# Optimization experiments

Hardware: AMD Instinct MI355X
Metric: run time of the kernel (lower is better)

Reference implementation:

```python
import jax, jax.numpy as jnp
import numpy as np

NUM_HEADS = 16
SRC_FACTS = 4


def setup_inputs() -> dict:
    key = jax.random.key(0)
    k1, k2, k3, k4, k5 = jax.random.split(key, 5)
    B, S, H, Dh = 16, 512, NUM_HEADS, 64  # B = batch(4) * src_facts(4)
    D = H * Dh  # d_model = 1024
    pre_q = jax.random.normal(k1, (B, S, H, Dh), dtype=jnp.float32)
    pre_v = jax.random.normal(k2, (B, S, H, Dh), dtype=jnp.float32)
    pre_k = jax.random.normal(k3, (B, S, H, Dh), dtype=jnp.float32)
    attn_mask = jax.random.randint(k4, (B, S, S), 0, 2).astype(jnp.int32)
    output_weights = jax.random.normal(k5, (D, D), dtype=jnp.float32) / np.float32(np.sqrt(D))
    return {
        "pre_q": pre_q,
        "pre_v": pre_v,
        "pre_k": pre_k,
        "attn_mask": attn_mask,
        "output_weights": output_weights,
        "out_seq_len": 512,
        "d_model": 1024,
    }


def reference(pre_q, pre_v, pre_k, attn_mask, output_weights, out_seq_len, d_model):
    B, Sq, H, Dh = pre_q.shape
    # Original: K.sqrt(cast(d_model) // num_heads) -> sqrt(head_dim)
    scale = jnp.sqrt(jnp.float32(float(d_model) // H))
    mask = attn_mask.astype(jnp.float32)[:, None]  # (B, 1, q, k) broadcast over heads
    # scores: (B, H, q, k)
    scores = jnp.einsum("bqhd,bkhd->bhqk", pre_q, pre_k) / scale
    # multiplicative pre-mask + additive -1e9 on masked slots
    scores = scores * mask + (1.0 - mask) * jnp.float32(-1e9)
    # softmax then multiplicative post-mask
    attn = jax.nn.softmax(scores, axis=-1) * mask
    heads = jnp.einsum("bhqk,bkhd->bqhd", attn, pre_v)  # (B, q, H, Dh)
    out = heads.reshape(B, Sq, H * Dh) @ output_weights  # (B, q, d_model)
    return out.reshape(-1, SRC_FACTS, out_seq_len, d_model)
```

## Files before the change

kernel.cpp:

```cpp
#include <hip/hip_runtime.h>
#include <hip/hip_bf16.h>


typedef __bf16 bf16;
typedef bf16 bf16x8 __attribute__((ext_vector_type(8)));
typedef bf16 bf16x4 __attribute__((ext_vector_type(4)));
typedef float floatx4 __attribute__((ext_vector_type(4)));
typedef float floatx16 __attribute__((ext_vector_type(16)));
typedef unsigned short ushort8 __attribute__((ext_vector_type(8)));
typedef unsigned long long u64;

#define MFMA32(A, B, C)  __builtin_amdgcn_mfma_f32_16x16x32_bf16((A), (B), (C), 0, 0, 0)
#define MFMA32x32(A, B, C) __builtin_amdgcn_mfma_f32_32x32x16_bf16((A), (B), (C), 0, 0, 0)

namespace {
constexpr int S   = 512;
constexpr int H   = 16;
constexpr int Dh  = 64;
constexpr int D   = 1024;
constexpr int LDT = 72;
constexpr size_t QN = (size_t)16 * S * H * Dh;
constexpr size_t WN = (size_t)D * D;
}

__device__ __forceinline__ float fexp2(float x) {
#if defined(__HIP_DEVICE_COMPILE__) && __has_builtin(__builtin_amdgcn_exp2f)
    return __builtin_amdgcn_exp2f(x);
#else
    return exp2f(x);
#endif
}

__device__ __forceinline__ int sbfe1(unsigned bits, int bit) {
    return ((int)(bits << (31 - bit))) >> 31;
}

__global__ __launch_bounds__(256)
void prep_kernel(const float* __restrict__ Kf, const float* __restrict__ Vf,
                 const float* __restrict__ Wf, const int* __restrict__ Mg,
                 bf16* __restrict__ Kc, bf16* __restrict__ Vt,
                 bf16* __restrict__ Wt, u64* __restrict__ MB)
{
    __shared__ bf16 Ts[64 * LDT];
    const int blk = blockIdx.x, tid = threadIdx.x;

    if (blk < 4096) {
        const int i = blk * 256 + tid;
        const float* fs = Kf + (size_t)i * 8;
        bf16x8 v;
#pragma unroll
        for (int j = 0; j < 8; ++j) v[j] = (bf16)fs[j];
        *(bf16x8*)(Kc + (size_t)i * 8) = v;
    } else if (blk < 6144) {
        const int bk2 = blk - 4096;
        const int bh  = bk2 >> 3, st = bk2 & 7;
        const int b   = bh >> 4, h = bh & 15;
        const int r   = tid >> 2, c = (tid & 3) * 16;
        const float* src = Vf + ((size_t)((b * S + st * 64 + r) * H + h)) * Dh + c;
#pragma unroll
        for (int i = 0; i < 16; ++i)
            Ts[(c + i) * LDT + r] = (bf16)src[i];
        __syncthreads();
        bf16* dst = Vt + ((size_t)bh * 64 + r) * S + st * 64 + c;
        *(ushort8*)dst       = *(const ushort8*)&Ts[r * LDT + c];
        *(ushort8*)(dst + 8) = *(const ushort8*)&Ts[r * LDT + c + 8];
    } else if (blk < 6400) {
        const int bk2 = blk - 6144;
        const int nb  = bk2 & 15, kb = bk2 >> 4;
        const int r   = tid >> 2, c = (tid & 3) * 16;
        const float* src = Wf + (size_t)(kb * 64 + r) * D + nb * 64 + c;
#pragma unroll
        for (int i = 0; i < 16; ++i)
            Ts[(c + i) * LDT + r] = (bf16)src[i];
        __syncthreads();
        bf16* dst = Wt + (size_t)(nb * 64 + r) * D + kb * 64 + c;
        *(ushort8*)dst       = *(const ushort8*)&Ts[r * LDT + c];
        *(ushort8*)(dst + 8) = *(const ushort8*)&Ts[r * LDT + c + 8];
    } else {
        const int bk2  = blk - 6400;
        const int lane = tid & 63;
        const int idx4 = bk2 * 4 + (tid >> 6);
        const int row  = idx4 >> 1;
        const int half = idx4 & 1;
#pragma unroll
        for (int r = 0; r < 4; ++r) {
            int mv = Mg[(size_t)row * 512 + half * 256 + r * 64 + lane];
            u64 bm = __ballot(mv != 0);
            if (lane == 0) MB[(size_t)row * 8 + half * 4 + r] = bm;
        }
    }
}

__global__ __launch_bounds__(256, 4)
void attn_kernel(const float* __restrict__ Qg, const bf16* __restrict__ Kc,
                 const bf16* __restrict__ Vtg, const u64* __restrict__ MB,
                 bf16* __restrict__ heads)
{
    __shared__ bf16 Ks[64 * LDT];
    __shared__ bf16 Vt[64 * LDT];

    const int tid  = threadIdx.x;
    const int lane = tid & 63;
    const int wave = tid >> 6;
    const int l31  = lane & 31;
    const int half = lane >> 5;

    const int blk = blockIdx.x;
    const int h   = blk & 15;
    const int qt  = (blk >> 4) & 3;
    const int b   = blk >> 6;
    const int qw  = qt * 128 + wave * 32;

    constexpr float QSCL = 0.125f * 1.44269504088896340736f;
    bf16x8 aq[4];
    {
        const float* qb = Qg + ((size_t)((b * S + qw + l31) * H + h)) * Dh + half * 8;
#pragma unroll
        for (int ds = 0; ds < 4; ++ds) {
            floatx4 f0 = *(const floatx4*)(qb + ds * 16);
            floatx4 f1 = *(const floatx4*)(qb + ds * 16 + 4);
#pragma unroll
            for (int j = 0; j < 4; ++j) {
                aq[ds][j]     = (bf16)(f0[j] * QSCL);
                aq[ds][j + 4] = (bf16)(f1[j] * QSCL);
            }
        }
    }

    float rsum = 0.f;
    floatx16 O[2];
#pragma unroll
    for (int dt = 0; dt < 2; ++dt)
#pragma unroll
        for (int i = 0; i < 16; ++i) O[dt][i] = 0.f;

    const u64* mbrow = MB + ((size_t)b * S + qw + l31) * 8;
    const bf16* vplane = Vtg + (size_t)(b * 16 + h) * 64 * S;

    const int sr = tid >> 2, sc_ = (tid & 3) * 16;
    const int kperm = (sr & 0x33) | ((sr & 4) << 1) | ((sr & 8) >> 1);

    for (int kt = 0; kt < 8; ++kt) {
        const int kb = kt * 64;
        const bf16* ksrc = Kc + ((size_t)((b * S + kb + kperm) * H + h)) * Dh + sc_;
        const bf16* vsrc = vplane + (size_t)sr * S + kb + sc_;
        ushort8 k0 = *(const ushort8*)ksrc;
        ushort8 k1 = *(const ushort8*)(ksrc + 8);
        ushort8 v0 = *(const ushort8*)vsrc;
        ushort8 v1 = *(const ushort8*)(vsrc + 8);
        u64 m64 = mbrow[kt];

        __syncthreads();
        *(ushort8*)&Ks[sr * LDT + sc_]     = k0;
        *(ushort8*)&Ks[sr * LDT + sc_ + 8] = k1;
        *(ushort8*)&Vt[sr * LDT + sc_]     = v0;
        *(ushort8*)&Vt[sr * LDT + sc_ + 8] = v1;
        __syncthreads();

        bf16x8 pB[4];
#pragma unroll
        for (int t = 0; t < 2; ++t) {
            floatx16 acc;
#pragma unroll
            for (int i = 0; i < 16; ++i) acc[i] = 0.f;
#pragma unroll
            for (int ds = 0; ds < 4; ++ds) {
                bf16x8 ak = *(const bf16x8*)&Ks[(t * 32 + l31) * LDT + ds * 16 + half * 8];
                acc = MFMA32x32(ak, aq[ds], acc);
            }
            const unsigned w = (unsigned)(m64 >> (t * 32 + half * 8));
#pragma unroll
            for (int r = 0; r < 16; ++r) {
                float e = fexp2(acc[r]);
                int sx = sbfe1(w, (r >> 3) * 16 + (r & 7));
                float p = __uint_as_float(__float_as_uint(e) & (unsigned)sx);
                rsum += p;
                pB[t * 2 + (r >> 3)][r & 7] = (bf16)p;
            }
        }

#pragma unroll
        for (int dt = 0; dt < 2; ++dt)
#pragma unroll
            for (int s_ = 0; s_ < 4; ++s_) {
                bf16x8 av = *(const bf16x8*)&Vt[(dt * 32 + l31) * LDT + s_ * 16 + half * 8];
                O[dt] = MFMA32x32(av, pB[s_], O[dt]);
            }
    }

    rsum += __shfl_xor(rsum, 32, 64);
    const float inv = (rsum > 0.f) ? (1.f / rsum) : 0.f;

    bf16* hrow = heads + ((size_t)((b * S + qw + l31) * H + h)) * Dh;
#pragma unroll
    for (int dt = 0; dt < 2; ++dt) {
#pragma unroll
        for (int g = 0; g < 4; ++g) {
            bf16x4 h4;
#pragma unroll
            for (int j = 0; j < 4; ++j) h4[j] = (bf16)(O[dt][g * 4 + j] * inv);
            *(bf16x4*)&hrow[dt * 32 + g * 8 + half * 4] = h4;
        }
    }
}

__global__ __launch_bounds__(256)
void proj_kernel(const bf16* __restrict__ A, const bf16* __restrict__ Wt,
                 float* __restrict__ out)
{
    __shared__ bf16 As[128 * LDT];
    __shared__ bf16 Ws[128 * LDT];

    const int tid  = threadIdx.x;
    const int lane = tid & 63;
    const int wave = tid >> 6;
    const int l15  = lane & 15;
    const int quad = lane >> 4;

    const int nb = blockIdx.x & 7;
    const int mb = blockIdx.x >> 3;
    const int mbase = mb * 128, nbase = nb * 128;
    const int wm = (wave & 1) * 64, wn = (wave >> 1) * 64;

    const int pr = tid >> 1, pc = (tid & 1) * 32;

    floatx4 O[4][4];
#pragma unroll
    for (int mt = 0; mt < 4; ++mt)
#pragma unroll
        for (int nt = 0; nt < 4; ++nt) O[mt][nt] = floatx4{0.f, 0.f, 0.f, 0.f};

    for (int kt = 0; kt < 16; ++kt) {
        const int kb = kt * 64;
        const bf16* asrc = A  + (size_t)(mbase + pr) * D + kb + pc;
        const bf16* wsrc = Wt + (size_t)(nbase + pr) * D + kb + pc;
        ushort8 a0 = *(const ushort8*)asrc;
        ushort8 a1 = *(const ushort8*)(asrc + 8);
        ushort8 a2 = *(const ushort8*)(asrc + 16);
        ushort8 a3 = *(const ushort8*)(asrc + 24);
        ushort8 w0 = *(const ushort8*)wsrc;
        ushort8 w1 = *(const ushort8*)(wsrc + 8);
        ushort8 w2 = *(const ushort8*)(wsrc + 16);
        ushort8 w3 = *(const ushort8*)(wsrc + 24);

        __syncthreads();
        *(ushort8*)&As[pr * LDT + pc]      = a0;
        *(ushort8*)&As[pr * LDT + pc + 8]  = a1;
        *(ushort8*)&As[pr * LDT + pc + 16] = a2;
        *(ushort8*)&As[pr * LDT + pc + 24] = a3;
        *(ushort8*)&Ws[pr * LDT + pc]      = w0;
        *(ushort8*)&Ws[pr * LDT + pc + 8]  = w1;
        *(ushort8*)&Ws[pr * LDT + pc + 16] = w2;
        *(ushort8*)&Ws[pr * LDT + pc + 24] = w3;
        __syncthreads();

        bf16x8 fa[4][2];
#pragma unroll
        for (int mt = 0; mt < 4; ++mt) {
            fa[mt][0] = *(const bf16x8*)&As[(wm + mt * 16 + l15) * LDT + quad * 8];
            fa[mt][1] = *(const bf16x8*)&As[(wm + mt * 16 + l15) * LDT + quad * 8 + 32];
        }
#pragma unroll
        for (int nt = 0; nt < 4; ++nt) {
            bf16x8 fb0 = *(const bf16x8*)&Ws[(wn + nt * 16 + l15) * LDT + quad * 8];
            bf16x8 fb1 = *(const bf16x8*)&Ws[(wn + nt * 16 + l15) * LDT + quad * 8 + 32];
#pragma unroll
            for (int mt = 0; mt < 4; ++mt) {
                O[mt][nt] = MFMA32(fa[mt][0], fb0, O[mt][nt]);
                O[mt][nt] = MFMA32(fa[mt][1], fb1, O[mt][nt]);
            }
        }
    }

#pragma unroll
    for (int mt = 0; mt < 4; ++mt) {
#pragma unroll
        for (int nt = 0; nt < 4; ++nt) {
#pragma unroll
            for (int reg = 0; reg < 4; ++reg) {
                const int m = mbase + wm + mt * 16 + quad * 4 + reg;
                const int n = nbase + wn + nt * 16 + l15;
                out[(size_t)m * D + n] = O[mt][nt][reg];
            }
        }
    }
}

extern "C" void kernel_launch(void* const* d_in, const int* in_sizes, int n_in,
                              void* d_out, int out_size, void* d_ws, size_t ws_size,
                              hipStream_t stream)
{
    const float* pre_q = (const float*)d_in[0];
    const float* pre_v = (const float*)d_in[1];
    const float* pre_k = (const float*)d_in[2];
    const int*   mask  = (const int*)d_in[3];
    const float* Wg    = (const float*)d_in[4];
    float* out = (float*)d_out;

    bf16* Kc    = (bf16*)d_ws;
    bf16* Vt    = Kc + QN;
    bf16* Wt    = Vt + QN;
    bf16* heads = Wt + WN;
    u64*  MB    = (u64*)(heads + QN);

    prep_kernel<<<10496, 256, 0, stream>>>(pre_k, pre_v, Wg, mask, Kc, Vt, Wt, MB);
    attn_kernel<<<1024, 256, 0, stream>>>(pre_q, Kc, Vt, MB, heads);
    proj_kernel<<<512, 256, 0, stream>>>(heads, Wt, out);
}
```

Measured before the change: 211.6 us.

## Double-buffer K/V tiles in attention and batch more work per prep block

The attention kernel now keeps two LDS buffers for K and V. It prefetches the next tile into registers two iterations ahead, so each iteration needs one barrier instead of two and global loads overlap the MFMA work. The prep kernel has each block convert four K chunks with vectorized float4 loads, and each mask wave ballots 16 row-segments, which cuts the grid from 10496 to 4352 blocks. The cost is double the LDS per block and higher register pressure, which could reduce occupancy under launch_bounds(256,4).

```diff
diff --git a/kernel.cpp b/kernel.cpp
--- a/kernel.cpp
+++ b/kernel.cpp
@@ -10,7 +10,7 @@
 typedef unsigned short ushort8 __attribute__((ext_vector_type(8)));
 typedef unsigned long long u64;
 
-#define MFMA32(A, B, C)  __builtin_amdgcn_mfma_f32_16x16x32_bf16((A), (B), (C), 0, 0, 0)
+#define MFMA32(A, B, C)    __builtin_amdgcn_mfma_f32_16x16x32_bf16((A), (B), (C), 0, 0, 0)
 #define MFMA32x32(A, B, C) __builtin_amdgcn_mfma_f32_32x32x16_bf16((A), (B), (C), 0, 0, 0)
 
 namespace {
@@ -44,15 +44,27 @@
     __shared__ bf16 Ts[64 * LDT];
     const int blk = blockIdx.x, tid = threadIdx.x;
 
-    if (blk < 4096) {
-        const int i = blk * 256 + tid;
-        const float* fs = Kf + (size_t)i * 8;
-        bf16x8 v;
-#pragma unroll
-        for (int j = 0; j < 8; ++j) v[j] = (bf16)fs[j];
-        *(bf16x8*)(Kc + (size_t)i * 8) = v;
-    } else if (blk < 6144) {
-        const int bk2 = blk - 4096;
+    if (blk < 1024) {
+        const int c0 = blk * 1024 + tid;
+        floatx4 f[4][2];
+#pragma unroll
+        for (int k = 0; k < 4; ++k) {
+            const float* fs = Kf + (size_t)(c0 + k * 256) * 8;
+            f[k][0] = *(const floatx4*)fs;
+            f[k][1] = *(const floatx4*)(fs + 4);
+        }
+#pragma unroll
+        for (int k = 0; k < 4; ++k) {
+            bf16x8 v;
+#pragma unroll
+            for (int j = 0; j < 4; ++j) {
+                v[j]     = (bf16)f[k][0][j];
+                v[j + 4] = (bf16)f[k][1][j];
+            }
+            *(bf16x8*)(Kc + (size_t)(c0 + k * 256) * 8) = v;
+        }
+    } else if (blk < 3072) {
+        const int bk2 = blk - 1024;
         const int bh  = bk2 >> 3, st = bk2 & 7;
         const int b   = bh >> 4, h = bh & 15;
         const int r   = tid >> 2, c = (tid & 3) * 16;
@@ -64,8 +76,8 @@
         bf16* dst = Vt + ((size_t)bh * 64 + r) * S + st * 64 + c;
         *(ushort8*)dst       = *(const ushort8*)&Ts[r * LDT + c];
         *(ushort8*)(dst + 8) = *(const ushort8*)&Ts[r * LDT + c + 8];
-    } else if (blk < 6400) {
-        const int bk2 = blk - 6144;
+    } else if (blk < 3328) {
+        const int bk2 = blk - 3072;
         const int nb  = bk2 & 15, kb = bk2 >> 4;
         const int r   = tid >> 2, c = (tid & 3) * 16;
         const float* src = Wf + (size_t)(kb * 64 + r) * D + nb * 64 + c;
@@ -77,16 +89,28 @@
         *(ushort8*)dst       = *(const ushort8*)&Ts[r * LDT + c];
         *(ushort8*)(dst + 8) = *(const ushort8*)&Ts[r * LDT + c + 8];
     } else {
-        const int bk2  = blk - 6400;
+        const int bk2  = blk - 3328;
         const int lane = tid & 63;
-        const int idx4 = bk2 * 4 + (tid >> 6);
-        const int row  = idx4 >> 1;
-        const int half = idx4 & 1;
-#pragma unroll
-        for (int r = 0; r < 4; ++r) {
-            int mv = Mg[(size_t)row * 512 + half * 256 + r * 64 + lane];
-            u64 bm = __ballot(mv != 0);
-            if (lane == 0) MB[(size_t)row * 8 + half * 4 + r] = bm;
+        const int wv   = tid >> 6;
+        const int u0   = bk2 * 16 + wv * 4;
+        int mv[4][4];
+#pragma unroll
+        for (int u = 0; u < 4; ++u) {
+            const int idx4 = u0 + u;
+            const int row = idx4 >> 1, hf = idx4 & 1;
+#pragma unroll
+            for (int r = 0; r < 4; ++r)
+                mv[u][r] = Mg[(size_t)row * 512 + hf * 256 + r * 64 + lane];
+        }
+#pragma unroll
+        for (int u = 0; u < 4; ++u) {
+            const int idx4 = u0 + u;
+            const int row = idx4 >> 1, hf = idx4 & 1;
+#pragma unroll
+            for (int r = 0; r < 4; ++r) {
+                u64 bm = __ballot(mv[u][r] != 0);
+                if (lane == 0) MB[(size_t)row * 8 + hf * 4 + r] = bm;
+            }
         }
     }
 }
@@ -96,8 +120,8 @@
                  const bf16* __restrict__ Vtg, const u64* __restrict__ MB,
                  bf16* __restrict__ heads)
 {
-    __shared__ bf16 Ks[64 * LDT];
-    __shared__ bf16 Vt[64 * LDT];
+    __shared__ bf16 Ks[2][64 * LDT];
+    __shared__ bf16 Vs[2][64 * LDT];
 
     const int tid  = threadIdx.x;
     const int lane = tid & 63;
@@ -140,22 +164,48 @@
     const int sr = tid >> 2, sc_ = (tid & 3) * 16;
     const int kperm = (sr & 0x33) | ((sr & 4) << 1) | ((sr & 8) >> 1);
 
+    const bf16* ksrc0 = Kc + ((size_t)((b * S + kperm) * H + h)) * Dh + sc_;
+    const bf16* vsrc0 = vplane + (size_t)sr * S + sc_;
+    const size_t kstep = (size_t)64 * H * Dh;
+
+    ushort8 k0 = *(const ushort8*)ksrc0;
+    ushort8 k1 = *(const ushort8*)(ksrc0 + 8);
+    ushort8 v0 = *(const ushort8*)vsrc0;
+    ushort8 v1 = *(const ushort8*)(vsrc0 + 8);
+    u64 mcur = mbrow[0];
+    *(ushort8*)&Ks[0][sr * LDT + sc_]     = k0;
+    *(ushort8*)&Ks[0][sr * LDT + sc_ + 8] = k1;
+    *(ushort8*)&Vs[0][sr * LDT + sc_]     = v0;
+    *(ushort8*)&Vs[0][sr * LDT + sc_ + 8] = v1;
+    k0 = *(const ushort8*)(ksrc0 + kstep);
+    k1 = *(const ushort8*)(ksrc0 + kstep + 8);
+    v0 = *(const ushort8*)(vsrc0 + 64);
+    v1 = *(const ushort8*)(vsrc0 + 64 + 8);
+    u64 mnext = mbrow[1];
+
+    int p = 0;
     for (int kt = 0; kt < 8; ++kt) {
-        const int kb = kt * 64;
-        const bf16* ksrc = Kc + ((size_t)((b * S + kb + kperm) * H + h)) * Dh + sc_;
-        const bf16* vsrc = vplane + (size_t)sr * S + kb + sc_;
-        ushort8 k0 = *(const ushort8*)ksrc;
-        ushort8 k1 = *(const ushort8*)(ksrc + 8);
-        ushort8 v0 = *(const ushort8*)vsrc;
-        ushort8 v1 = *(const ushort8*)(vsrc + 8);
-        u64 m64 = mbrow[kt];
-
-        __syncthreads();
-        *(ushort8*)&Ks[sr * LDT + sc_]     = k0;
-        *(ushort8*)&Ks[sr * LDT + sc_ + 8] = k1;
-        *(ushort8*)&Vt[sr * LDT + sc_]     = v0;
-        *(ushort8*)&Vt[sr * LDT + sc_ + 8] = v1;
-        __syncthreads();
+        __syncthreads();
+        if (kt < 7) {
+            *(ushort8*)&Ks[p ^ 1][sr * LDT + sc_]     = k0;
+            *(ushort8*)&Ks[p ^ 1][sr * LDT + sc_ + 8] = k1;
+            *(ushort8*)&Vs[p ^ 1][sr * LDT + sc_]     = v0;
+            *(ushort8*)&Vs[p ^ 1][sr * LDT + sc_ + 8] = v1;
+        }
+        const u64 mk = mcur;
+        mcur = mnext;
+        if (kt < 6) {
+            const bf16* ks = ksrc0 + (size_t)(kt + 2) * kstep;
+            const bf16* vs = vsrc0 + (kt + 2) * 64;
+            k0 = *(const ushort8*)ks;
+            k1 = *(const ushort8*)(ks + 8);
+            v0 = *(const ushort8*)vs;
+            v1 = *(const ushort8*)(vs + 8);
+            mnext = mbrow[kt + 2];
+        }
+
+        const bf16* __restrict__ ksp = Ks[p];
+        const bf16* __restrict__ vsp = Vs[p];
 
         bf16x8 pB[4];
 #pragma unroll
@@ -165,17 +215,17 @@
             for (int i = 0; i < 16; ++i) acc[i] = 0.f;
 #pragma unroll
             for (int ds = 0; ds < 4; ++ds) {
-                bf16x8 ak = *(const bf16x8*)&Ks[(t * 32 + l31) * LDT + ds * 16 + half * 8];
+                bf16x8 ak = *(const bf16x8*)&ksp[(t * 32 + l31) * LDT + ds * 16 + half * 8];
                 acc = MFMA32x32(ak, aq[ds], acc);
             }
-            const unsigned w = (unsigned)(m64 >> (t * 32 + half * 8));
+            const unsigned w = (unsigned)(mk >> (t * 32 + half * 8));
 #pragma unroll
             for (int r = 0; r < 16; ++r) {
                 float e = fexp2(acc[r]);
                 int sx = sbfe1(w, (r >> 3) * 16 + (r & 7));
-                float p = __uint_as_float(__float_as_uint(e) & (unsigned)sx);
-                rsum += p;
-                pB[t * 2 + (r >> 3)][r & 7] = (bf16)p;
+                float pv = __uint_as_float(__float_as_uint(e) & (unsigned)sx);
+                rsum += pv;
+                pB[t * 2 + (r >> 3)][r & 7] = (bf16)pv;
             }
         }
 
@@ -183,9 +233,10 @@
         for (int dt = 0; dt < 2; ++dt)
 #pragma unroll
             for (int s_ = 0; s_ < 4; ++s_) {
-                bf16x8 av = *(const bf16x8*)&Vt[(dt * 32 + l31) * LDT + s_ * 16 + half * 8];
+                bf16x8 av = *(const bf16x8*)&vsp[(dt * 32 + l31) * LDT + s_ * 16 + half * 8];
                 O[dt] = MFMA32x32(av, pB[s_], O[dt]);
             }
+        p ^= 1;
     }
 
     rsum += __shfl_xor(rsum, 32, 64);
@@ -303,7 +354,7 @@
     bf16* heads = Wt + WN;
     u64*  MB    = (u64*)(heads + QN);
 
-    prep_kernel<<<10496, 256, 0, stream>>>(pre_k, pre_v, Wg, mask, Kc, Vt, Wt, MB);
+    prep_kernel<<<4352, 256, 0, stream>>>(pre_k, pre_v, Wg, mask, Kc, Vt, Wt, MB);
     attn_kernel<<<1024, 256, 0, stream>>>(pre_q, Kc, Vt, MB, heads);
     proj_kernel<<<512, 256, 0, stream>>>(heads, Wt, out);
 }
```

Measured after the change: 213.1 us. Within noise of the previous version (+0.7%).

## Use direct global-to-LDS loads in projection and batch loads in prep kernel

Applied to the files above, without the earlier changes.

The projection GEMM now stages A and W tiles with global_load_lds (direct global-to-shared copies) using a 32-wide K tile, which removes the register round-trip and the padded LDS layout. The prep kernel makes each block convert four K chunks with vectorized float4 loads and build four mask ballots per wave, which cuts the grid size. It also XOR-swizzles the transpose scratch to avoid LDS bank conflicts. The trade-offs are more K iterations and syncs in the GEMM, no double buffering, and the unpadded 32-wide LDS rows may see bank conflicts on fragment reads.

```diff
diff --git a/kernel.cpp b/kernel.cpp
--- a/kernel.cpp
+++ b/kernel.cpp
@@ -10,7 +10,7 @@
 typedef unsigned short ushort8 __attribute__((ext_vector_type(8)));
 typedef unsigned long long u64;
 
-#define MFMA32(A, B, C)  __builtin_amdgcn_mfma_f32_16x16x32_bf16((A), (B), (C), 0, 0, 0)
+#define MFMA32(A, B, C)    __builtin_amdgcn_mfma_f32_16x16x32_bf16((A), (B), (C), 0, 0, 0)
 #define MFMA32x32(A, B, C) __builtin_amdgcn_mfma_f32_32x32x16_bf16((A), (B), (C), 0, 0, 0)
 
 namespace {
@@ -35,6 +35,16 @@
     return ((int)(bits << (31 - bit))) >> 31;
 }
 
+__device__ __forceinline__ void gload16(const bf16* g, bf16* ldsbase, int lane) {
+#if __has_builtin(__builtin_amdgcn_global_load_lds)
+    __builtin_amdgcn_global_load_lds(
+        (__attribute__((address_space(1))) void*)(g),
+        (__attribute__((address_space(3))) void*)(ldsbase), 16, 0, 0);
+#else
+    *(ushort8*)(ldsbase + lane * 8) = *(const ushort8*)g;
+#endif
+}
+
 __global__ __launch_bounds__(256)
 void prep_kernel(const float* __restrict__ Kf, const float* __restrict__ Vf,
                  const float* __restrict__ Wf, const int* __restrict__ Mg,
@@ -44,49 +54,75 @@
     __shared__ bf16 Ts[64 * LDT];
     const int blk = blockIdx.x, tid = threadIdx.x;
 
-    if (blk < 4096) {
-        const int i = blk * 256 + tid;
-        const float* fs = Kf + (size_t)i * 8;
-        bf16x8 v;
-#pragma unroll
-        for (int j = 0; j < 8; ++j) v[j] = (bf16)fs[j];
-        *(bf16x8*)(Kc + (size_t)i * 8) = v;
-    } else if (blk < 6144) {
-        const int bk2 = blk - 4096;
+    if (blk < 1024) {
+        const int c0 = blk * 1024 + tid;
+        floatx4 f[4][2];
+#pragma unroll
+        for (int k = 0; k < 4; ++k) {
+            const float* fs = Kf + (size_t)(c0 + k * 256) * 8;
+            f[k][0] = *(const floatx4*)fs;
+            f[k][1] = *(const floatx4*)(fs + 4);
+        }
+#pragma unroll
+        for (int k = 0; k < 4; ++k) {
+            bf16x8 v;
+#pragma unroll
+            for (int j = 0; j < 4; ++j) {
+                v[j]     = (bf16)f[k][0][j];
+                v[j + 4] = (bf16)f[k][1][j];
+            }
+            *(bf16x8*)(Kc + (size_t)(c0 + k * 256) * 8) = v;
+        }
+    } else if (blk < 3072) {
+        const int bk2 = blk - 1024;
         const int bh  = bk2 >> 3, st = bk2 & 7;
         const int b   = bh >> 4, h = bh & 15;
         const int r   = tid >> 2, c = (tid & 3) * 16;
         const float* src = Vf + ((size_t)((b * S + st * 64 + r) * H + h)) * Dh + c;
 #pragma unroll
         for (int i = 0; i < 16; ++i)
-            Ts[(c + i) * LDT + r] = (bf16)src[i];
+            Ts[(c + i) * LDT + (r ^ ((c + i) & 48))] = (bf16)src[i];
         __syncthreads();
         bf16* dst = Vt + ((size_t)bh * 64 + r) * S + st * 64 + c;
-        *(ushort8*)dst       = *(const ushort8*)&Ts[r * LDT + c];
-        *(ushort8*)(dst + 8) = *(const ushort8*)&Ts[r * LDT + c + 8];
-    } else if (blk < 6400) {
-        const int bk2 = blk - 6144;
+        const int rb = r * LDT + (c ^ (r & 48));
+        *(ushort8*)dst       = *(const ushort8*)&Ts[rb];
+        *(ushort8*)(dst + 8) = *(const ushort8*)&Ts[rb + 8];
+    } else if (blk < 3328) {
+        const int bk2 = blk - 3072;
         const int nb  = bk2 & 15, kb = bk2 >> 4;
         const int r   = tid >> 2, c = (tid & 3) * 16;
         const float* src = Wf + (size_t)(kb * 64 + r) * D + nb * 64 + c;
 #pragma unroll
         for (int i = 0; i < 16; ++i)
-            Ts[(c + i) * LDT + r] = (bf16)src[i];
+            Ts[(c + i) * LDT + (r ^ ((c + i) & 48))] = (bf16)src[i];
         __syncthreads();
         bf16* dst = Wt + (size_t)(nb * 64 + r) * D + kb * 64 + c;
-        *(ushort8*)dst       = *(const ushort8*)&Ts[r * LDT + c];
-        *(ushort8*)(dst + 8) = *(const ushort8*)&Ts[r * LDT + c + 8];
+        const int rb = r * LDT + (c ^ (r & 48));
+        *(ushort8*)dst       = *(const ushort8*)&Ts[rb];
+        *(ushort8*)(dst + 8) = *(const ushort8*)&Ts[rb + 8];
     } else {
-        const int bk2  = blk - 6400;
+        const int bk2  = blk - 3328;
         const int lane = tid & 63;
-        const int idx4 = bk2 * 4 + (tid >> 6);
-        const int row  = idx4 >> 1;
-        const int half = idx4 & 1;
-#pragma unroll
-        for (int r = 0; r < 4; ++r) {
-            int mv = Mg[(size_t)row * 512 + half * 256 + r * 64 + lane];
-            u64 bm = __ballot(mv != 0);
-            if (lane == 0) MB[(size_t)row * 8 + half * 4 + r] = bm;
+        const int wv   = tid >> 6;
+        const int u0   = bk2 * 16 + wv * 4;
+        int mv[4][4];
+#pragma unroll
+        for (int u = 0; u < 4; ++u) {
+            const int idx4 = u0 + u;
+            const int row = idx4 >> 1, hf = idx4 & 1;
+#pragma unroll
+            for (int r = 0; r < 4; ++r)
+                mv[u][r] = Mg[(size_t)row * 512 + hf * 256 + r * 64 + lane];
+        }
+#pragma unroll
+        for (int u = 0; u < 4; ++u) {
+            const int idx4 = u0 + u;
+            const int row = idx4 >> 1, hf = idx4 & 1;
+#pragma unroll
+            for (int r = 0; r < 4; ++r) {
+                u64 bm = __ballot(mv[u][r] != 0);
+                if (lane == 0) MB[(size_t)row * 8 + hf * 4 + r] = bm;
+            }
         }
     }
 }
@@ -208,8 +244,8 @@
 void proj_kernel(const bf16* __restrict__ A, const bf16* __restrict__ Wt,
                  float* __restrict__ out)
 {
-    __shared__ bf16 As[128 * LDT];
-    __shared__ bf16 Ws[128 * LDT];
+    __shared__ bf16 As[128 * 32];
+    __shared__ bf16 Ws[128 * 32];
 
     const int tid  = threadIdx.x;
     const int lane = tid & 63;
@@ -222,7 +258,9 @@
     const int mbase = mb * 128, nbase = nb * 128;
     const int wm = (wave & 1) * 64, wn = (wave >> 1) * 64;
 
-    const int pr = tid >> 1, pc = (tid & 1) * 32;
+    const int ch0  = wave * 2;
+    const int srow = lane >> 2;
+    const int scol = (lane & 3) * 8;
 
     floatx4 O[4][4];
 #pragma unroll
@@ -230,45 +268,27 @@
 #pragma unroll
         for (int nt = 0; nt < 4; ++nt) O[mt][nt] = floatx4{0.f, 0.f, 0.f, 0.f};
 
-    for (int kt = 0; kt < 16; ++kt) {
-        const int kb = kt * 64;
-        const bf16* asrc = A  + (size_t)(mbase + pr) * D + kb + pc;
-        const bf16* wsrc = Wt + (size_t)(nbase + pr) * D + kb + pc;
-        ushort8 a0 = *(const ushort8*)asrc;
-        ushort8 a1 = *(const ushort8*)(asrc + 8);
-        ushort8 a2 = *(const ushort8*)(asrc + 16);
-        ushort8 a3 = *(const ushort8*)(asrc + 24);
-        ushort8 w0 = *(const ushort8*)wsrc;
-        ushort8 w1 = *(const ushort8*)(wsrc + 8);
-        ushort8 w2 = *(const ushort8*)(wsrc + 16);
-        ushort8 w3 = *(const ushort8*)(wsrc + 24);
-
-        __syncthreads();
-        *(ushort8*)&As[pr * LDT + pc]      = a0;
-        *(ushort8*)&As[pr * LDT + pc + 8]  = a1;
-        *(ushort8*)&As[pr * LDT + pc + 16] = a2;
-        *(ushort8*)&As[pr * LDT + pc + 24] = a3;
-        *(ushort8*)&Ws[pr * LDT + pc]      = w0;
-        *(ushort8*)&Ws[pr * LDT + pc + 8]  = w1;
-        *(ushort8*)&Ws[pr * LDT + pc + 16] = w2;
-        *(ushort8*)&Ws[pr * LDT + pc + 24] = w3;
-        __syncthreads();
-
-        bf16x8 fa[4][2];
-#pragma unroll
-        for (int mt = 0; mt < 4; ++mt) {
-            fa[mt][0] = *(const bf16x8*)&As[(wm + mt * 16 + l15) * LDT + quad * 8];
-            fa[mt][1] = *(const bf16x8*)&As[(wm + mt * 16 + l15) * LDT + quad * 8 + 32];
-        }
+    for (int kt = 0; kt < 32; ++kt) {
+        const int kb = kt * 32;
+        if (kt) __syncthreads();
+
+        gload16(A  + (size_t)(mbase + ch0 * 16      + srow) * D + kb + scol, As + ch0 * 512,       lane);
+        gload16(A  + (size_t)(mbase + (ch0 + 1) * 16 + srow) * D + kb + scol, As + (ch0 + 1) * 512, lane);
+        gload16(Wt + (size_t)(nbase + ch0 * 16      + srow) * D + kb + scol, Ws + ch0 * 512,       lane);
+        gload16(Wt + (size_t)(nbase + (ch0 + 1) * 16 + srow) * D + kb + scol, Ws + (ch0 + 1) * 512, lane);
+
+        __syncthreads();
+
+        bf16x8 fa[4];
+#pragma unroll
+        for (int mt = 0; mt < 4; ++mt)
+            fa[mt] = *(const bf16x8*)&As[(wm + mt * 16 + l15) * 32 + quad * 8];
 #pragma unroll
         for (int nt = 0; nt < 4; ++nt) {
-            bf16x8 fb0 = *(const bf16x8*)&Ws[(wn + nt * 16 + l15) * LDT + quad * 8];
-            bf16x8 fb1 = *(const bf16x8*)&Ws[(wn + nt * 16 + l15) * LDT + quad * 8 + 32];
-#pragma unroll
-            for (int mt = 0; mt < 4; ++mt) {
-                O[mt][nt] = MFMA32(fa[mt][0], fb0, O[mt][nt]);
-                O[mt][nt] = MFMA32(fa[mt][1], fb1, O[mt][nt]);
-            }
+            bf16x8 fb = *(const bf16x8*)&Ws[(wn + nt * 16 + l15) * 32 + quad * 8];
+#pragma unroll
+            for (int mt = 0; mt < 4; ++mt)
+                O[mt][nt] = MFMA32(fa[mt], fb, O[mt][nt]);
         }
     }
 
@@ -303,7 +323,7 @@
     bf16* heads = Wt + WN;
     u64*  MB    = (u64*)(heads + QN);
 
-    prep_kernel<<<10496, 256, 0, stream>>>(pre_k, pre_v, Wg, mask, Kc, Vt, Wt, MB);
+    prep_kernel<<<4352, 256, 0, stream>>>(pre_k, pre_v, Wg, mask, Kc, Vt, Wt, MB);
     attn_kernel<<<1024, 256, 0, stream>>>(pre_q, Kc, Vt, MB, heads);
     proj_kernel<<<512, 256, 0, stream>>>(heads, Wt, out);
 }
```

After: 209.4 us. No clear change (-1.0%).
